# Performance work log

Hardware: AMD Instinct MI355X
Metric: run time of the kernel (lower is better)

The kernel has to match this reference:

```python
import jax, jax.numpy as jnp
import numpy as np

GROUPS = 8   # GroupNorm groups used by create_pat_conv*_blocks(..., groups=8)
EPS = 1e-5
K = 20       # num_neighbor


def group_norm(x, gamma, beta):
    # x: [B, C, ...spatial]
    B, C = x.shape[0], x.shape[1]
    shape = x.shape
    xg = x.reshape(B, GROUPS, C // GROUPS, -1)
    m = xg.mean(axis=(2, 3), keepdims=True)
    v = ((xg - m) ** 2).mean(axis=(2, 3), keepdims=True)
    xg = (xg - m) * jax.lax.rsqrt(v + EPS)
    x = xg.reshape(shape)
    bshape = (1, C) + (1,) * (len(shape) - 2)
    return x * gamma.reshape(bshape) + beta.reshape(bshape)


def conv_block(x, w, b, gamma, beta):
    # pointwise (kernel-size 1) conv + GroupNorm + ELU, works for 1d and 2d spatial
    y = jnp.einsum('oc,bc...->bo...', w, x) + b.reshape((1, -1) + (1,) * (x.ndim - 2))
    return jax.nn.elu(group_norm(y, gamma, beta))


def knn_graph(points, k):
    # points: [B, 3, N] -> neighbor coords [B, 3, N, k] (self included, dilation=1)
    sq = jnp.sum(points * points, axis=1)                      # [B, N]
    inner = jnp.einsum('bci,bcj->bij', points, points)         # [B, N, N]
    dist = sq[:, :, None] + sq[:, None, :] - 2.0 * inner       # squared pairwise dist
    _, idx = jax.lax.top_k(-dist, k)                           # [B, N, k] smallest dists
    neighbors = jnp.take_along_axis(points[:, :, None, :], idx[:, None, :, :], axis=3)
    return neighbors                                           # [B, 3, N, k]


def setup_inputs() -> dict:
    key = jax.random.key(0)
    B, N = 4, 8192
    dims1 = [6, 32, 64]
    dims2 = [64, 512, 1024]
    keys = iter(jax.random.split(key, 32))
    inp = {"points": jax.random.normal(next(keys), (B, 3, N), dtype=jnp.float32)}
    for tag, dims in (("p1", dims1), ("p2", dims2)):
        for i in range(len(dims) - 1):
            cin, cout = dims[i], dims[i + 1]
            inp[f"{tag}_w{i}"] = jax.random.normal(next(keys), (cout, cin), dtype=jnp.float32) / np.float32(np.sqrt(cin))
            inp[f"{tag}_b{i}"] = jnp.zeros((cout,), dtype=jnp.float32)
            inp[f"{tag}_g{i}"] = jnp.ones((cout,), dtype=jnp.float32)
            inp[f"{tag}_beta{i}"] = jnp.zeros((cout,), dtype=jnp.float32)
    return inp


def reference(points, p1_w0, p1_b0, p1_g0, p1_beta0, p1_w1, p1_b1, p1_g1, p1_beta1,
              p2_w0, p2_b0, p2_g0, p2_beta0, p2_w1, p2_b1, p2_g1, p2_beta1):
    neighbors = knn_graph(points, K)                             # [B, 3, N, K]
    center = jnp.broadcast_to(points[:, :, :, None], neighbors.shape)
    x = jnp.concatenate([center, neighbors - center], axis=1)   # [B, 6, N, K]
    x = conv_block(x, p1_w0, p1_b0, p1_g0, p1_beta0)            # [B, 32, N, K]
    x = conv_block(x, p1_w1, p1_b1, p1_g1, p1_beta1)            # [B, 64, N, K]
    x = jnp.max(x, axis=2)                                      # [B, 64, K] (faithful to source: max over dim=2)
    x = conv_block(x, p2_w0, p2_b0, p2_g0, p2_beta0)            # [B, 512, K]
    x = conv_block(x, p2_w1, p2_b1, p2_g1, p2_beta1)            # [B, 1024, K]
    return x
```

## Files before the change

kernel.cpp:

```cpp
#include <hip/hip_runtime.h>
#include <math.h>

#define NPTS   8192
#define BATCH  4
#define KNN    20
#define NKTOT  (NPTS*KNN)
#define EPS    1e-5f
#define QC2    16

typedef float v2f __attribute__((ext_vector_type(2)));

__device__ __forceinline__ float elu(float x) { return x > 0.0f ? x : expm1f(x); }
__device__ __forceinline__ float eluf(float x) { return x > 0.0f ? x : __expf(x) - 1.0f; }
__device__ __forceinline__ v2f splat2(float x) { v2f v; v.x = x; v.y = x; return v; }
__device__ __forceinline__ float rfl(float x) {
    return __uint_as_float(__builtin_amdgcn_readfirstlane(__float_as_uint(x)));
}

__device__ __forceinline__ unsigned fenc(float f) {
    unsigned b = __float_as_uint(f);
    return b ^ ((unsigned)(((int)b) >> 31) | 0x80000000u);
}
__device__ __forceinline__ float fdec(unsigned u) {
    unsigned b = (u & 0x80000000u) ? (u ^ 0x80000000u) : ~u;
    return __uint_as_float(b);
}

__global__ __launch_bounds__(256) void prep_kernel(const float* __restrict__ points,
                                                   float4* __restrict__ pts4,
                                                   float* __restrict__ zeroreg,
                                                   unsigned* __restrict__ minenc)
{
    const int t = blockIdx.x * 256 + threadIdx.x;
    const int b = t >> 13, n = t & (NPTS - 1);
    const float* px = points + b * 3 * NPTS;
    float x = px[n], y = px[NPTS + n], z = px[2 * NPTS + n];
    pts4[t] = make_float4(x, y, z, -0.5f * (x * x + y * y + z * z));
    if (t < 18176) zeroreg[t] = 0.f;
    if (t < 5120)  minenc[t] = 0xFFFFFFFFu;
}

__global__ __launch_bounds__(256, 8) void knn_kernel(const float4* __restrict__ pts4,
                                                     int* __restrict__ idx_out)
{
    __shared__ unsigned long long queue[32][QC2];
    __shared__ float smaxs[4][8][64];
    __shared__ float gates[8];
    __shared__ int qcnt[32];

    const int tid  = threadIdx.x;
    const int lane = tid & 63;
    const int wv   = tid >> 6;
    const int b    = blockIdx.x >> 10;
    const int q0   = (blockIdx.x & 1023) * 8;
    const float4* pb = pts4 + b * NPTS;
    const int cbase = wv * (NPTS / 4);

    if (tid < 32) qcnt[tid] = 0;

    float qx[8], qy[8], qz[8];
    v2f smax2[8];
#pragma unroll
    for (int q = 0; q < 8; ++q) {
        float4 qp = pb[q0 + q];
        qx[q] = rfl(qp.x); qy[q] = rfl(qp.y); qz[q] = rfl(qp.z);
        smax2[q] = splat2(-INFINITY);
    }

#pragma unroll 4
    for (int t = 0; t < NPTS / 4 / 128; ++t) {
        float4 p0 = pb[cbase + t * 128 + 2 * lane];
        float4 p1 = pb[cbase + t * 128 + 2 * lane + 1];
        v2f px = { p0.x, p1.x }, py = { p0.y, p1.y };
        v2f pz = { p0.z, p1.z }, pw = { p0.w, p1.w };
#pragma unroll
        for (int q = 0; q < 8; ++q) {
            v2f sv = __builtin_elementwise_fma(splat2(qx[q]), px,
                     __builtin_elementwise_fma(splat2(qy[q]), py,
                     __builtin_elementwise_fma(splat2(qz[q]), pz, pw)));
            smax2[q] = __builtin_elementwise_max(smax2[q], sv);
        }
    }
#pragma unroll
    for (int q = 0; q < 8; ++q) smaxs[wv][q][lane] = fmaxf(smax2[q].x, smax2[q].y);
    __syncthreads();

#pragma unroll
    for (int qq = 0; qq < 2; ++qq) {
        const int q = wv * 2 + qq;
        float v = fmaxf(fmaxf(smaxs[0][q][lane], smaxs[1][q][lane]),
                        fmaxf(smaxs[2][q][lane], smaxs[3][q][lane]));
#pragma unroll
        for (int k = 2; k <= 64; k <<= 1)
#pragma unroll
            for (int j = k >> 1; j >= 1; j >>= 1) {
                float o = __shfl_xor(v, j);
                bool up = ((lane & k) == 0);
                bool keepmin = (((lane & j) == 0) == up);
                v = keepmin ? fminf(v, o) : fmaxf(v, o);
            }
        float m = __shfl(v, 44);
        if (lane == 0) gates[q] = m - 1e-4f - 1e-5f * fabsf(m);
    }
    __syncthreads();
    float sgate[8];
#pragma unroll
    for (int q = 0; q < 8; ++q) sgate[q] = gates[q];

    for (int t = 0; t < NPTS / 4 / 128; ++t) {
        float4 p0 = pb[cbase + t * 128 + 2 * lane];
        float4 p1 = pb[cbase + t * 128 + 2 * lane + 1];
        v2f px = { p0.x, p1.x }, py = { p0.y, p1.y };
        v2f pz = { p0.z, p1.z }, pw = { p0.w, p1.w };
        const int jb = cbase + t * 128 + 2 * lane;
#pragma unroll
        for (int q = 0; q < 8; ++q) {
            v2f sv = __builtin_elementwise_fma(splat2(qx[q]), px,
                     __builtin_elementwise_fma(splat2(qy[q]), py,
                     __builtin_elementwise_fma(splat2(qz[q]), pz, pw)));
            if (fmaxf(sv.x, sv.y) >= sgate[q]) {
#pragma unroll
                for (int h = 0; h < 2; ++h) {
                    float svh = h ? sv.y : sv.x;
                    if (svh >= sgate[q]) {
                        int slot = atomicAdd(&qcnt[wv * 8 + q], 1);
                        if (slot < QC2) {
                            unsigned long long key =
                                ((unsigned long long)fenc(svh) << 32)
                                | (unsigned)(NPTS - 1 - (jb + h));
                            queue[wv * 8 + q][slot] = key;
                        }
                    }
                }
            }
        }
    }
    __syncthreads();

#pragma unroll
    for (int qq = 0; qq < 2; ++qq) {
        const int q = wv * 2 + qq;
        int c0 = qcnt[0 * 8 + q];  c0 = c0 < QC2 ? c0 : QC2;
        int c1 = qcnt[1 * 8 + q];  c1 = c1 < QC2 ? c1 : QC2;
        int c2 = qcnt[2 * 8 + q];  c2 = c2 < QC2 ? c2 : QC2;
        int c3 = qcnt[3 * 8 + q];  c3 = c3 < QC2 ? c3 : QC2;
        int b1 = c0, b2 = c0 + c1, b3 = c0 + c1 + c2, b4 = b3 + c3;
        unsigned long long key = 0ull;
        if (lane < b1)      key = queue[0 * 8 + q][lane];
        else if (lane < b2) key = queue[1 * 8 + q][lane - b1];
        else if (lane < b3) key = queue[2 * 8 + q][lane - b2];
        else if (lane < b4) key = queue[3 * 8 + q][lane - b3];
#pragma unroll
        for (int k = 2; k <= 64; k <<= 1)
#pragma unroll
            for (int j = k >> 1; j >= 1; j >>= 1) {
                unsigned long long o = __shfl_xor(key, j);
                bool up = ((lane & k) == 0);
                bool keepmax = (((lane & j) == 0) == up);
                bool omax = o > key;
                key = (keepmax == omax) ? o : key;
            }
        if (lane < KNN)
            idx_out[(b * KNN + lane) * NPTS + (q0 + q)] =
                NPTS - 1 - (int)(unsigned)(key & 0xFFFFFFFFu);
    }
}

__global__ __launch_bounds__(256) void moments_x_kernel(const float4* __restrict__ pts4,
                                                        const int* __restrict__ idx,
                                                        float* __restrict__ sums1p)
{
    const int b  = blockIdx.x / 80;
    const int r0 = (blockIdx.x - b * 80) * 2048;
    const float4* pb = pts4 + b * NPTS;
    const int* ib = idx + b * NKTOT;

    float v[27];
#pragma unroll
    for (int i = 0; i < 27; ++i) v[i] = 0.f;

    for (int e = 0; e < 8; ++e) {
        const int id = r0 + e * 256 + threadIdx.x;
        const int n = id & (NPTS - 1);
        const int j = ib[id];
        float4 c4 = pb[n];
        float4 e4 = pb[j];
        float x[6] = { c4.x, c4.y, c4.z, e4.x - c4.x, e4.y - c4.y, e4.z - c4.z };
        int p = 6;
#pragma unroll
        for (int d = 0; d < 6; ++d) {
            v[d] += x[d];
#pragma unroll
            for (int ee = d; ee < 6; ++ee) v[p++] += x[d] * x[ee];
        }
    }
#pragma unroll
    for (int i = 0; i < 27; ++i)
        for (int o = 32; o > 0; o >>= 1) v[i] += __shfl_xor(v[i], o);

    __shared__ float red[4][27];
    const int lane = threadIdx.x & 63, w = threadIdx.x >> 6;
    if (lane == 0)
#pragma unroll
        for (int i = 0; i < 27; ++i) red[w][i] = v[i];
    __syncthreads();
    if (threadIdx.x < 27) {
        float acc = red[0][threadIdx.x] + red[1][threadIdx.x] + red[2][threadIdx.x] + red[3][threadIdx.x];
        int slot = blockIdx.x & 63;
        atomicAdd(&sums1p[(slot * BATCH + b) * 27 + threadIdx.x], acc);
    }
}

__global__ void finalize1_kernel(const float* __restrict__ sums1p,
                                 const float* __restrict__ w1, const float* __restrict__ b1,
                                 const float* __restrict__ g1, const float* __restrict__ beta1,
                                 float* __restrict__ w1f)
{
    __shared__ float S[BATCH][27];
    const int t = threadIdx.x;
    if (t < 108) {
        int b = t / 27, i = t % 27;
        float acc = 0.f;
        for (int s = 0; s < 64; ++s) acc += sums1p[(s * BATCH + b) * 27 + i];
        S[b][i] = acc;
    }
    __syncthreads();
    const int b = t >> 5, c = t & 31;
    const float invS = 1.0f / (float)NKTOT;
    float Ex[6], M[6][6];
#pragma unroll
    for (int d = 0; d < 6; ++d) Ex[d] = S[b][d] * invS;
    int p = 6;
#pragma unroll
    for (int d = 0; d < 6; ++d)
#pragma unroll
        for (int e = d; e < 6; ++e) { float v = S[b][p++] * invS; M[d][e] = v; M[e][d] = v; }
    const int g = c >> 2;
    float msum = 0.f, qsum = 0.f;
    for (int cc = g * 4; cc < g * 4 + 4; ++cc) {
        float w[6];
#pragma unroll
        for (int d = 0; d < 6; ++d) w[d] = w1[cc * 6 + d];
        float dotEx = 0.f;
#pragma unroll
        for (int d = 0; d < 6; ++d) dotEx += w[d] * Ex[d];
        float Ey = dotEx + b1[cc];
        float Ey2 = 0.f;
#pragma unroll
        for (int d = 0; d < 6; ++d)
#pragma unroll
            for (int e = 0; e < 6; ++e) Ey2 += w[d] * w[e] * M[d][e];
        Ey2 += 2.0f * b1[cc] * dotEx + b1[cc] * b1[cc];
        msum += Ey; qsum += Ey2;
    }
    float m = msum * 0.25f;
    float var = qsum * 0.25f - m * m;
    float inv = rsqrtf(var + EPS);
    float s = g1[c] * inv;
    float tt = s * (b1[c] - m) + beta1[c];
    float* o = w1f + (b * 32 + c) * 8;
#pragma unroll
    for (int d = 0; d < 6; ++d) o[d] = s * w1[c * 6 + d];
    o[6] = tt; o[7] = 0.f;
}

__global__ __launch_bounds__(256, 3) void fused_main_kernel(
    const float4* __restrict__ pts4, const int* __restrict__ idxb,
    const float* __restrict__ w1f, const float* __restrict__ w2, const float* __restrict__ b2,
    float* __restrict__ sums2p, unsigned int* __restrict__ maxenc, unsigned int* __restrict__ minenc)
{
    __shared__ __align__(16) float w2t[32 * 64];
    __shared__ __align__(16) float z1s[32 * 256];
    __shared__ __align__(16) float4 w1s4[64];
    __shared__ float b2s[64];
    __shared__ float redmx[256], redmn[256], sqred[64];

    const int t   = threadIdx.x;
    const int blk = blockIdx.x;
    const int nc  = blk & 15;
    const int k   = (blk >> 4) % 20;
    const int b   = blk / 320;

    for (int i = t; i < 512; i += 256) {
        float4 v = ((const float4*)w2)[i];
        int c = i >> 3, kq = (i & 7) * 4;
        w2t[(kq + 0) * 64 + c] = v.x; w2t[(kq + 1) * 64 + c] = v.y;
        w2t[(kq + 2) * 64 + c] = v.z; w2t[(kq + 3) * 64 + c] = v.w;
    }
    if (t < 64) { w1s4[t] = ((const float4*)w1f)[b * 64 + t]; b2s[t] = b2[t]; }

    const int wvi = t >> 6;
    const int cg8 = t & 7;
    const int n0  = (t >> 3) * 8;
    const int c0  = cg8 * 8;
    const float4* pb = pts4 + b * NPTS;
    const int nbase = nc * 512;
    const int* idxrow = idxb + (b * KNN + k) * NPTS;

    float mx[8], mn[8];
#pragma unroll
    for (int ci = 0; ci < 8; ++ci) { mx[ci] = -INFINITY; mn[ci] = INFINITY; }
    float gs = 0.f, gq = 0.f;

    for (int ph = 0; ph < 2; ++ph) {
        const int n = nbase + ph * 256 + t;
        const int j = idxrow[n];
        float4 c4 = pb[n];
        float4 e4 = pb[j];
        float x0[6] = { c4.x, c4.y, c4.z, e4.x - c4.x, e4.y - c4.y, e4.z - c4.z };

        __syncthreads();
#pragma unroll
        for (int c = 0; c < 32; ++c) {
            float4 wA = w1s4[c * 2 + 0];
            float4 wB = w1s4[c * 2 + 1];
            float z = wB.z;
            z = fmaf(wA.x, x0[0], z); z = fmaf(wA.y, x0[1], z); z = fmaf(wA.z, x0[2], z);
            z = fmaf(wA.w, x0[3], z); z = fmaf(wB.x, x0[4], z); z = fmaf(wB.y, x0[5], z);
            z1s[c * 256 + t] = eluf(z);
        }
        __syncthreads();

        float acc[8][8];
#pragma unroll
        for (int ci = 0; ci < 8; ++ci) {
            float bb = b2s[c0 + ci];
#pragma unroll
            for (int pj = 0; pj < 8; ++pj) acc[ci][pj] = bb;
        }
#pragma unroll
        for (int kk = 0; kk < 32; ++kk) {
            float4 a0 = *(const float4*)&w2t[kk * 64 + c0];
            float4 a1 = *(const float4*)&w2t[kk * 64 + c0 + 4];
            float4 z0 = *(const float4*)&z1s[kk * 256 + n0];
            float4 z1v = *(const float4*)&z1s[kk * 256 + n0 + 4];
            float avv[8] = { a0.x, a0.y, a0.z, a0.w, a1.x, a1.y, a1.z, a1.w };
            float zvv[8] = { z0.x, z0.y, z0.z, z0.w, z1v.x, z1v.y, z1v.z, z1v.w };
#pragma unroll
            for (int ci = 0; ci < 8; ++ci)
#pragma unroll
                for (int pj = 0; pj < 8; ++pj) acc[ci][pj] = fmaf(avv[ci], zvv[pj], acc[ci][pj]);
        }
#pragma unroll
        for (int ci = 0; ci < 8; ++ci)
#pragma unroll
            for (int pj = 0; pj < 8; ++pj) {
                float v = acc[ci][pj];
                gs += v; gq = fmaf(v, v, gq);
                mx[ci] = fmaxf(mx[ci], v); mn[ci] = fminf(mn[ci], v);
            }
    }

#pragma unroll
    for (int m = 8; m <= 32; m <<= 1) {
#pragma unroll
        for (int ci = 0; ci < 8; ++ci) {
            mx[ci] = fmaxf(mx[ci], __shfl_xor(mx[ci], m));
            mn[ci] = fminf(mn[ci], __shfl_xor(mn[ci], m));
        }
        gs += __shfl_xor(gs, m);
        gq += __shfl_xor(gq, m);
    }
    if ((t & 63) < 8) {
        const int l = t & 7;
#pragma unroll
        for (int ci = 0; ci < 8; ++ci) {
            redmx[wvi * 64 + l * 8 + ci] = mx[ci];
            redmn[wvi * 64 + l * 8 + ci] = mn[ci];
        }
        sqred[(wvi * 8 + l) * 2 + 0] = gs;
        sqred[(wvi * 8 + l) * 2 + 1] = gq;
    }
    __syncthreads();
    if (t < 64) {
        float m = fmaxf(fmaxf(redmx[t], redmx[64 + t]), fmaxf(redmx[128 + t], redmx[192 + t]));
        atomicMax(&maxenc[(b * 64 + t) * KNN + k], fenc(m));
    } else if (t < 128) {
        int c = t - 64;
        float m = fminf(fminf(redmn[c], redmn[64 + c]), fminf(redmn[128 + c], redmn[192 + c]));
        atomicMin(&minenc[(b * 64 + c) * KNN + k], fenc(m));
    } else if (t < 144) {
        int i2 = t - 128, g = i2 >> 1, w = i2 & 1;
        float v = 0.f;
#pragma unroll
        for (int wv2 = 0; wv2 < 4; ++wv2)
            v += sqred[(wv2 * 8 + g) * 2 + w];
        int slot = blk & 63;
        atomicAdd(&sums2p[((slot * BATCH + b) * 8 + g) * 2 + w], v);
    }
}

__global__ void build_m1_kernel(const float* __restrict__ sums2p,
                                const unsigned int* __restrict__ maxenc,
                                const unsigned int* __restrict__ minenc,
                                const float* __restrict__ gamma, const float* __restrict__ beta,
                                float* __restrict__ m1)
{
    const int t = blockIdx.x * 256 + threadIdx.x;
    const int b = t / 1280;
    const int r = t - b * 1280;
    const int c = r / 20;
    const int g = c >> 3;
    float s = 0.f, q = 0.f;
    for (int sl = 0; sl < 64; ++sl) {
        s += sums2p[((sl * BATCH + b) * 8 + g) * 2 + 0];
        q += sums2p[((sl * BATCH + b) * 8 + g) * 2 + 1];
    }
    const float cnt = 8.0f * (float)NKTOT;
    float m = s / cnt;
    float var = q / cnt - m * m;
    float inv = rsqrtf(var + EPS);
    float sc = gamma[c] * inv;
    float tt = beta[c] - sc * m;
    float y = (sc >= 0.f) ? fdec(maxenc[t]) : fdec(minenc[t]);
    m1[t] = elu(sc * y + tt);
}

template <int CIN, int SLOTS>
__global__ void p2_gemm_kernel(const float* __restrict__ zin, const float* __restrict__ w,
                               const float* __restrict__ bias, float* __restrict__ yout,
                               float* __restrict__ sumsp, int chans_per_group)
{
    const int t = blockIdx.x * 256 + threadIdx.x;
    const int per_b = (gridDim.x * 256) / BATCH;
    const int b = t / per_b;
    const int r = t - b * per_b;
    const int o = r / 20;
    const int k = r - o * 20;
    const float* zb = zin + b * CIN * 20;
    const float* wrow = w + o * CIN;
    float acc = bias[o];
    for (int c = 0; c < CIN; c += 4) {
        float4 wv = *(const float4*)&wrow[c];
        acc += wv.x * zb[(c + 0) * 20 + k] + wv.y * zb[(c + 1) * 20 + k]
             + wv.z * zb[(c + 2) * 20 + k] + wv.w * zb[(c + 3) * 20 + k];
    }
    yout[t] = acc;

    __shared__ float ls[16];
    if (threadIdx.x < 16) ls[threadIdx.x] = 0.f;
    __syncthreads();
    const int g = o / chans_per_group;
    atomicAdd(&ls[g * 2 + 0], acc);
    atomicAdd(&ls[g * 2 + 1], acc * acc);
    __syncthreads();
    if (threadIdx.x < 16) {
        int slot = blockIdx.x & (SLOTS - 1);
        atomicAdd(&sumsp[(slot * BATCH + b) * 16 + threadIdx.x], ls[threadIdx.x]);
    }
}

template <int SLOTS>
__global__ void p2_finalize_kernel(const float* __restrict__ y, const float* __restrict__ sumsp,
                                   const float* __restrict__ gamma, const float* __restrict__ beta,
                                   float* __restrict__ z, int chans_per_group, float cnt)
{
    const int t = blockIdx.x * 256 + threadIdx.x;
    const int per_b = (gridDim.x * 256) / BATCH;
    const int b = t / per_b;
    const int r = t - b * per_b;
    const int o = r / 20;
    const int g = o / chans_per_group;
    float s = 0.f, q = 0.f;
    for (int sl = 0; sl < SLOTS; ++sl) {
        s += sumsp[(sl * BATCH + b) * 16 + g * 2 + 0];
        q += sumsp[(sl * BATCH + b) * 16 + g * 2 + 1];
    }
    float m = s / cnt;
    float var = q / cnt - m * m;
    float inv = rsqrtf(var + EPS);
    float v = gamma[o] * inv * (y[t] - m) + beta[o];
    z[t] = elu(v);
}

extern "C" void kernel_launch(void* const* d_in, const int* in_sizes, int n_in,
                              void* d_out, int out_size, void* d_ws, size_t ws_size,
                              hipStream_t stream)
{
    const float* points  = (const float*)d_in[0];
    const float* p1_w0   = (const float*)d_in[1];
    const float* p1_b0   = (const float*)d_in[2];
    const float* p1_g0   = (const float*)d_in[3];
    const float* p1_bt0  = (const float*)d_in[4];
    const float* p1_w1   = (const float*)d_in[5];
    const float* p1_b1   = (const float*)d_in[6];
    const float* p1_g1   = (const float*)d_in[7];
    const float* p1_bt1  = (const float*)d_in[8];
    const float* p2_w0   = (const float*)d_in[9];
    const float* p2_b0   = (const float*)d_in[10];
    const float* p2_g0   = (const float*)d_in[11];
    const float* p2_bt0  = (const float*)d_in[12];
    const float* p2_w1   = (const float*)d_in[13];
    const float* p2_b1   = (const float*)d_in[14];
    const float* p2_g1   = (const float*)d_in[15];
    const float* p2_bt1  = (const float*)d_in[16];
    float* out = (float*)d_out;

    float* ws = (float*)d_ws;
    int*      idx     = (int*)ws;
    float*    sums1p  = ws + 655360;
    float*    sums2p  = sums1p + 6912;
    float*    sumsAp  = sums2p + 4096;
    float*    sumsBp  = sumsAp + 1024;
    unsigned* maxenc  = (unsigned*)(sumsBp + 1024);
    unsigned* minenc  = maxenc + 5120;
    float*    w1f     = (float*)(minenc + 5120);
    float*    m1      = w1f + 1024;
    float*    yp2a    = m1 + 5120;
    float*    zp2a    = yp2a + 40960;
    float*    yp2b    = zp2a + 40960;
    float4*   pts4    = (float4*)yp2a;

    prep_kernel<<<128, 256, 0, stream>>>(points, pts4, sums1p, minenc);
    knn_kernel<<<4096, 256, 0, stream>>>(pts4, idx);
    moments_x_kernel<<<320, 256, 0, stream>>>(pts4, idx, sums1p);
    finalize1_kernel<<<1, 128, 0, stream>>>(sums1p, p1_w0, p1_b0, p1_g0, p1_bt0, w1f);
    fused_main_kernel<<<1280, 256, 0, stream>>>(pts4, idx, w1f, p1_w1, p1_b1,
                                                sums2p, maxenc, minenc);
    build_m1_kernel<<<20, 256, 0, stream>>>(sums2p, maxenc, minenc, p1_g1, p1_bt1, m1);
    p2_gemm_kernel<64, 16><<<160, 256, 0, stream>>>(m1, p2_w0, p2_b0, yp2a, sumsAp, 64);
    p2_finalize_kernel<16><<<160, 256, 0, stream>>>(yp2a, sumsAp, p2_g0, p2_bt0, zp2a, 64, 1280.0f);
    p2_gemm_kernel<512, 16><<<320, 256, 0, stream>>>(zp2a, p2_w1, p2_b1, yp2b, sumsBp, 128);
    p2_finalize_kernel<16><<<320, 256, 0, stream>>>(yp2b, sumsBp, p2_g1, p2_bt1, out, 128, 2560.0f);
}
```

Before: 258.5 us.

## Sort points by x and restrict KNN search to a window with exact fallback

Points are bucketed by x coordinate with a histogram plus scatter into sorted order. Each query block then scans a 3072-point window around its sorted position instead of all 8192 points. A per-query check compares the 20th-neighbour distance against the distance to the window's x edges, and any query that fails, or whose candidate queue overflowed, is recomputed by a full-scan fallback kernel. This cuts the brute-force distance work at the cost of extra sort kernels, gather indirection and a data-dependent fallback pass.

```diff
diff --git a/kernel.cpp b/kernel.cpp
--- a/kernel.cpp
+++ b/kernel.cpp
@@ -8,6 +8,12 @@
 #define EPS    1e-5f
 #define QC2    16
 
+#define WINW   3072
+#define WITR   (WINW/4/128)
+#define NBIN   1024
+#define BIN_LO (-4.5f)
+#define BIN_W  (9.0f/1024.0f)
+
 typedef float v2f __attribute__((ext_vector_type(2)));
 
 __device__ __forceinline__ float elu(float x) { return x > 0.0f ? x : expm1f(x); }
@@ -26,10 +32,16 @@
     return __uint_as_float(b);
 }
 
+__device__ __forceinline__ int xbin(float x) {
+    int bin = (int)floorf((x + 4.5f) * (1024.0f / 9.0f));
+    return bin < 0 ? 0 : (bin > NBIN - 1 ? NBIN - 1 : bin);
+}
+
 __global__ __launch_bounds__(256) void prep_kernel(const float* __restrict__ points,
                                                    float4* __restrict__ pts4,
                                                    float* __restrict__ zeroreg,
-                                                   unsigned* __restrict__ minenc)
+                                                   unsigned* __restrict__ minenc,
+                                                   unsigned* __restrict__ fcnt)
 {
     const int t = blockIdx.x * 256 + threadIdx.x;
     const int b = t >> 13, n = t & (NPTS - 1);
@@ -38,10 +50,54 @@
     pts4[t] = make_float4(x, y, z, -0.5f * (x * x + y * y + z * z));
     if (t < 18176) zeroreg[t] = 0.f;
     if (t < 5120)  minenc[t] = 0xFFFFFFFFu;
-}
-
-__global__ __launch_bounds__(256, 8) void knn_kernel(const float4* __restrict__ pts4,
-                                                     int* __restrict__ idx_out)
+    if (t < 4)     fcnt[t] = 0u;
+}
+
+__global__ __launch_bounds__(1024) void hist_kernel(const float* __restrict__ points,
+                                                    int* __restrict__ Pcur)
+{
+    __shared__ int h[NBIN];
+    __shared__ int sc[NBIN];
+    const int b = blockIdx.x;
+    const int t = threadIdx.x;
+    h[t] = 0;
+    __syncthreads();
+    const float* px = points + b * 3 * NPTS;
+    for (int i = t; i < NPTS; i += 1024)
+        atomicAdd(&h[xbin(px[i])], 1);
+    __syncthreads();
+    int v = h[t];
+    sc[t] = v;
+    __syncthreads();
+    for (int off = 1; off < NBIN; off <<= 1) {
+        int a = (t >= off) ? sc[t - off] : 0;
+        __syncthreads();
+        sc[t] += a;
+        __syncthreads();
+    }
+    Pcur[b * NBIN + t] = sc[t] - v;
+}
+
+__global__ __launch_bounds__(256) void scatter_kernel(const float4* __restrict__ pts4,
+                                                      int* __restrict__ Pcur,
+                                                      float4* __restrict__ psort,
+                                                      int* __restrict__ sidx,
+                                                      int* __restrict__ binof)
+{
+    const int t = blockIdx.x * 256 + threadIdx.x;
+    const int b = t >> 13, n = t & (NPTS - 1);
+    float4 p = pts4[t];
+    int bin = xbin(p.x);
+    int slot = atomicAdd(&Pcur[b * NBIN + bin], 1);
+    psort[b * NPTS + slot] = p;
+    sidx [b * NPTS + slot] = n;
+    binof[b * NPTS + slot] = bin;
+}
+
+__global__ __launch_bounds__(256, 8) void knn_win_kernel(
+    const float4* __restrict__ psort, const int* __restrict__ sidx,
+    const int* __restrict__ binof, int* __restrict__ idx_out,
+    unsigned* __restrict__ fcnt, int* __restrict__ flist)
 {
     __shared__ unsigned long long queue[32][QC2];
     __shared__ float smaxs[4][8][64];
@@ -52,25 +108,34 @@
     const int lane = tid & 63;
     const int wv   = tid >> 6;
     const int b    = blockIdx.x >> 10;
-    const int q0   = (blockIdx.x & 1023) * 8;
-    const float4* pb = pts4 + b * NPTS;
-    const int cbase = wv * (NPTS / 4);
+    const int oct  = blockIdx.x & 1023;
+    const int q0s  = oct * 8;
+    const float4* psb = psort + b * NPTS;
+    const int*    six = sidx  + b * NPTS;
+    const int*    bob = binof + b * NPTS;
+
+    int s = q0s + 4 - WINW / 2;
+    if (s < 0) s = 0;
+    if (s > NPTS - WINW) s = NPTS - WINW;
 
     if (tid < 32) qcnt[tid] = 0;
 
-    float qx[8], qy[8], qz[8];
+    float qx[8], qy[8], qz[8], q2[8];
     v2f smax2[8];
 #pragma unroll
     for (int q = 0; q < 8; ++q) {
-        float4 qp = pb[q0 + q];
+        float4 qp = psb[q0s + q];
         qx[q] = rfl(qp.x); qy[q] = rfl(qp.y); qz[q] = rfl(qp.z);
+        q2[q] = rfl(-(qp.w + qp.w));
         smax2[q] = splat2(-INFINITY);
     }
 
-#pragma unroll 4
-    for (int t = 0; t < NPTS / 4 / 128; ++t) {
-        float4 p0 = pb[cbase + t * 128 + 2 * lane];
-        float4 p1 = pb[cbase + t * 128 + 2 * lane + 1];
+    const int lbase = s + wv * 2 + lane * 8;
+
+#pragma unroll 3
+    for (int t = 0; t < WITR; ++t) {
+        float4 p0 = psb[lbase + t * 512];
+        float4 p1 = psb[lbase + t * 512 + 1];
         v2f px = { p0.x, p1.x }, py = { p0.y, p1.y };
         v2f pz = { p0.z, p1.z }, pw = { p0.w, p1.w };
 #pragma unroll
@@ -107,12 +172,12 @@
 #pragma unroll
     for (int q = 0; q < 8; ++q) sgate[q] = gates[q];
 
-    for (int t = 0; t < NPTS / 4 / 128; ++t) {
-        float4 p0 = pb[cbase + t * 128 + 2 * lane];
-        float4 p1 = pb[cbase + t * 128 + 2 * lane + 1];
+    for (int t = 0; t < WITR; ++t) {
+        const int jb = lbase + t * 512;
+        float4 p0 = psb[jb];
+        float4 p1 = psb[jb + 1];
         v2f px = { p0.x, p1.x }, py = { p0.y, p1.y };
         v2f pz = { p0.z, p1.z }, pw = { p0.w, p1.w };
-        const int jb = cbase + t * 128 + 2 * lane;
 #pragma unroll
         for (int q = 0; q < 8; ++q) {
             v2f sv = __builtin_elementwise_fma(splat2(qx[q]), px,
@@ -125,10 +190,10 @@
                     if (svh >= sgate[q]) {
                         int slot = atomicAdd(&qcnt[wv * 8 + q], 1);
                         if (slot < QC2) {
-                            unsigned long long key =
+                            int j = six[jb + h];
+                            queue[wv * 8 + q][slot] =
                                 ((unsigned long long)fenc(svh) << 32)
-                                | (unsigned)(NPTS - 1 - (jb + h));
-                            queue[wv * 8 + q][slot] = key;
+                                | (unsigned)(NPTS - 1 - j);
                         }
                     }
                 }
@@ -137,13 +202,21 @@
     }
     __syncthreads();
 
+    float xLe = (s == 0) ? -3.0e38f
+                         : (BIN_LO + (float)(bob[s] + 1) * BIN_W);
+    float xRe = (s == NPTS - WINW) ? 3.0e38f
+                         : (BIN_LO + (float)bob[s + WINW] * BIN_W);
+
 #pragma unroll
     for (int qq = 0; qq < 2; ++qq) {
         const int q = wv * 2 + qq;
-        int c0 = qcnt[0 * 8 + q];  c0 = c0 < QC2 ? c0 : QC2;
-        int c1 = qcnt[1 * 8 + q];  c1 = c1 < QC2 ? c1 : QC2;
-        int c2 = qcnt[2 * 8 + q];  c2 = c2 < QC2 ? c2 : QC2;
-        int c3 = qcnt[3 * 8 + q];  c3 = c3 < QC2 ? c3 : QC2;
+        int c0r = qcnt[0 * 8 + q], c1r = qcnt[1 * 8 + q];
+        int c2r = qcnt[2 * 8 + q], c3r = qcnt[3 * 8 + q];
+        const bool ovf = (c0r > QC2) || (c1r > QC2) || (c2r > QC2) || (c3r > QC2);
+        int c0 = c0r < QC2 ? c0r : QC2;
+        int c1 = c1r < QC2 ? c1r : QC2;
+        int c2 = c2r < QC2 ? c2r : QC2;
+        int c3 = c3r < QC2 ? c3r : QC2;
         int b1 = c0, b2 = c0 + c1, b3 = c0 + c1 + c2, b4 = b3 + c3;
         unsigned long long key = 0ull;
         if (lane < b1)      key = queue[0 * 8 + q][lane];
@@ -160,9 +233,160 @@
                 bool omax = o > key;
                 key = (keepmax == omax) ? o : key;
             }
+        const int oq = __builtin_amdgcn_readfirstlane(six[q0s + q]);
         if (lane < KNN)
-            idx_out[(b * KNN + lane) * NPTS + (q0 + q)] =
+            idx_out[(b * KNN + lane) * NPTS + oq] =
                 NPTS - 1 - (int)(unsigned)(key & 0xFFFFFFFFu);
+
+        unsigned long long k19 = __shfl(key, 19);
+        float s20 = fdec((unsigned)(k19 >> 32));
+        float d20 = fmaxf(q2[q] - 2.0f * s20, 0.0f);
+        float mg  = 1e-3f + 1e-3f * d20;
+        float dL  = qx[q] - xLe;
+        float dR  = xRe - qx[q];
+        bool ok = !ovf && dL > 0.0f && dR > 0.0f
+                  && (d20 + mg < dL * dL) && (d20 + mg < dR * dR);
+        if (!ok && lane == 0) {
+            unsigned fs = atomicAdd(&fcnt[b], 1u);
+            if (fs < 8192u) flist[b * 8192 + fs] = oq;
+        }
+    }
+}
+
+__global__ __launch_bounds__(256, 8) void knn_fb_kernel(const float4* __restrict__ pts4,
+                                                        int* __restrict__ idx_out,
+                                                        const unsigned* __restrict__ fcnt,
+                                                        const int* __restrict__ flist)
+{
+    __shared__ unsigned long long queue[32][QC2];
+    __shared__ float smaxs[4][8][64];
+    __shared__ float gates[8];
+    __shared__ int qcnt[32];
+
+    const int tid  = threadIdx.x;
+    const int lane = tid & 63;
+    const int wv   = tid >> 6;
+    const int bb   = blockIdx.x & 3;
+    unsigned cnt = fcnt[bb];
+    if (cnt > 8192u) cnt = 8192u;
+    const float4* pb = pts4 + bb * NPTS;
+    const int* fl = flist + bb * 8192;
+    const int cbase = wv * (NPTS / 4);
+    const int tstep = gridDim.x >> 2;
+
+    for (int task = blockIdx.x >> 2; task * 8 < (int)cnt; task += tstep) {
+        int qn8[8];
+        float qx[8], qy[8], qz[8];
+        v2f smax2[8];
+        if (tid < 32) qcnt[tid] = 0;
+#pragma unroll
+        for (int q = 0; q < 8; ++q) {
+            int e = task * 8 + q;
+            if (e >= (int)cnt) e = (int)cnt - 1;
+            qn8[q] = __builtin_amdgcn_readfirstlane(fl[e]);
+            float4 qp = pb[qn8[q]];
+            qx[q] = rfl(qp.x); qy[q] = rfl(qp.y); qz[q] = rfl(qp.z);
+            smax2[q] = splat2(-INFINITY);
+        }
+
+#pragma unroll 4
+        for (int t = 0; t < NPTS / 4 / 128; ++t) {
+            float4 p0 = pb[cbase + t * 128 + 2 * lane];
+            float4 p1 = pb[cbase + t * 128 + 2 * lane + 1];
+            v2f px = { p0.x, p1.x }, py = { p0.y, p1.y };
+            v2f pz = { p0.z, p1.z }, pw = { p0.w, p1.w };
+#pragma unroll
+            for (int q = 0; q < 8; ++q) {
+                v2f sv = __builtin_elementwise_fma(splat2(qx[q]), px,
+                         __builtin_elementwise_fma(splat2(qy[q]), py,
+                         __builtin_elementwise_fma(splat2(qz[q]), pz, pw)));
+                smax2[q] = __builtin_elementwise_max(smax2[q], sv);
+            }
+        }
+#pragma unroll
+        for (int q = 0; q < 8; ++q) smaxs[wv][q][lane] = fmaxf(smax2[q].x, smax2[q].y);
+        __syncthreads();
+
+#pragma unroll
+        for (int qq = 0; qq < 2; ++qq) {
+            const int q = wv * 2 + qq;
+            float v = fmaxf(fmaxf(smaxs[0][q][lane], smaxs[1][q][lane]),
+                            fmaxf(smaxs[2][q][lane], smaxs[3][q][lane]));
+#pragma unroll
+            for (int k = 2; k <= 64; k <<= 1)
+#pragma unroll
+                for (int j = k >> 1; j >= 1; j >>= 1) {
+                    float o = __shfl_xor(v, j);
+                    bool up = ((lane & k) == 0);
+                    bool keepmin = (((lane & j) == 0) == up);
+                    v = keepmin ? fminf(v, o) : fmaxf(v, o);
+                }
+            float m = __shfl(v, 44);
+            if (lane == 0) gates[q] = m - 1e-4f - 1e-5f * fabsf(m);
+        }
+        __syncthreads();
+        float sgate[8];
+#pragma unroll
+        for (int q = 0; q < 8; ++q) sgate[q] = gates[q];
+
+        for (int t = 0; t < NPTS / 4 / 128; ++t) {
+            float4 p0 = pb[cbase + t * 128 + 2 * lane];
+            float4 p1 = pb[cbase + t * 128 + 2 * lane + 1];
+            v2f px = { p0.x, p1.x }, py = { p0.y, p1.y };
+            v2f pz = { p0.z, p1.z }, pw = { p0.w, p1.w };
+            const int jb = cbase + t * 128 + 2 * lane;
+#pragma unroll
+            for (int q = 0; q < 8; ++q) {
+                v2f sv = __builtin_elementwise_fma(splat2(qx[q]), px,
+                         __builtin_elementwise_fma(splat2(qy[q]), py,
+                         __builtin_elementwise_fma(splat2(qz[q]), pz, pw)));
+                if (fmaxf(sv.x, sv.y) >= sgate[q]) {
+#pragma unroll
+                    for (int h = 0; h < 2; ++h) {
+                        float svh = h ? sv.y : sv.x;
+                        if (svh >= sgate[q]) {
+                            int slot = atomicAdd(&qcnt[wv * 8 + q], 1);
+                            if (slot < QC2) {
+                                unsigned long long key =
+                                    ((unsigned long long)fenc(svh) << 32)
+                                    | (unsigned)(NPTS - 1 - (jb + h));
+                                queue[wv * 8 + q][slot] = key;
+                            }
+                        }
+                    }
+                }
+            }
+        }
+        __syncthreads();
+
+#pragma unroll
+        for (int qq = 0; qq < 2; ++qq) {
+            const int q = wv * 2 + qq;
+            int c0 = qcnt[0 * 8 + q];  c0 = c0 < QC2 ? c0 : QC2;
+            int c1 = qcnt[1 * 8 + q];  c1 = c1 < QC2 ? c1 : QC2;
+            int c2 = qcnt[2 * 8 + q];  c2 = c2 < QC2 ? c2 : QC2;
+            int c3 = qcnt[3 * 8 + q];  c3 = c3 < QC2 ? c3 : QC2;
+            int b1 = c0, b2 = c0 + c1, b3 = c0 + c1 + c2, b4 = b3 + c3;
+            unsigned long long key = 0ull;
+            if (lane < b1)      key = queue[0 * 8 + q][lane];
+            else if (lane < b2) key = queue[1 * 8 + q][lane - b1];
+            else if (lane < b3) key = queue[2 * 8 + q][lane - b2];
+            else if (lane < b4) key = queue[3 * 8 + q][lane - b3];
+#pragma unroll
+            for (int k = 2; k <= 64; k <<= 1)
+#pragma unroll
+                for (int j = k >> 1; j >= 1; j >>= 1) {
+                    unsigned long long o = __shfl_xor(key, j);
+                    bool up = ((lane & k) == 0);
+                    bool keepmax = (((lane & j) == 0) == up);
+                    bool omax = o > key;
+                    key = (keepmax == omax) ? o : key;
+                }
+            if (lane < KNN)
+                idx_out[(bb * KNN + lane) * NPTS + qn8[q]] =
+                    NPTS - 1 - (int)(unsigned)(key & 0xFFFFFFFFu);
+        }
+        __syncthreads();
     }
 }
 
@@ -510,9 +734,19 @@
     float*    zp2a    = yp2a + 40960;
     float*    yp2b    = zp2a + 40960;
     float4*   pts4    = (float4*)yp2a;
-
-    prep_kernel<<<128, 256, 0, stream>>>(points, pts4, sums1p, minenc);
-    knn_kernel<<<4096, 256, 0, stream>>>(pts4, idx);
+    float*    psortf  = yp2b + 81920;
+    float4*   psort4  = (float4*)psortf;
+    int*      sidx    = (int*)(psortf + 131072);
+    int*      binof   = sidx + 32768;
+    int*      Pcur    = binof + 32768 + 64;
+    unsigned* fcnt4   = (unsigned*)(Pcur + 4096);
+    int*      flist   = (int*)(fcnt4 + 64);
+
+    prep_kernel<<<128, 256, 0, stream>>>(points, pts4, sums1p, minenc, fcnt4);
+    hist_kernel<<<4, 1024, 0, stream>>>(points, Pcur);
+    scatter_kernel<<<128, 256, 0, stream>>>(pts4, Pcur, psort4, sidx, binof);
+    knn_win_kernel<<<4096, 256, 0, stream>>>(psort4, sidx, binof, idx, fcnt4, flist);
+    knn_fb_kernel<<<1024, 256, 0, stream>>>(pts4, idx, fcnt4, flist);
     moments_x_kernel<<<320, 256, 0, stream>>>(pts4, idx, sums1p);
     finalize1_kernel<<<1, 128, 0, stream>>>(sums1p, p1_w0, p1_b0, p1_g0, p1_bt0, w1f);
     fused_main_kernel<<<1280, 256, 0, stream>>>(pts4, idx, w1f, p1_w1, p1_b1,
```

After: 297.7 us. +15.2%, slower.
